# Optimization experiments

Hardware: AMD Instinct MI355X
Metric: run time of the kernel (lower is better)

The kernel has to match this reference:

```python
import jax, jax.numpy as jnp
from jax import lax
import numpy as np


def _chain(U, v, pos_seq):
    """Run the sequential Slater-determinant conditional-probability chain.
    U: (D, D) one-body density matrix P P^T.  v: (D, D) Jastrow matrix.
    pos_seq: (N,) int positions fed in order (replaces the sampling step,
    as in chainevaluate_amplitude).  Returns probs_all: (N, D).
    """
    D = U.shape[0]
    N = pos_seq.shape[0]
    diagU = jnp.diag(U)

    def step(carry, k):
        Xinv, Kpad, s = carry              # Xinv: (N,N) padded, Kpad: (N,) int, s: (D,)
        pos = pos_seq[k]
        # corr[pos'] = U[pos', K(:k)] @ Xinv(:k,:k) @ U[K(:k), pos']  for all pos'
        # padding is safe: rows/cols >= k of Xinv are zero.
        A = U[:, Kpad]                      # (D, N) gather of occupied columns
        corr = jnp.sum((A @ Xinv) * A, axis=1)          # (D,)
        unnorm = diagU - corr               # cond_prob_unnormalized (k=0: corr==0)
        probs_F = jnp.abs(unnorm / (N - k))  # Slater conditional prob
        probs_B = jnp.exp(-0.5 * s)          # Jastrow factor (k=0: s==0 -> ones)
        p = probs_F * probs_B
        probs = p / jnp.sum(p)
        # Sherman-Morrison rank-1 update of Xinv with the newly occupied site
        gg = 1.0 / unnorm[pos]
        uu = Xinv @ U[Kpad, pos]            # (N,)  zero beyond k
        vv = U[pos, Kpad] @ Xinv            # (N,)  (== uu since U symmetric)
        Xn = Xinv + gg * jnp.outer(uu, vv)
        Xn = Xn.at[k, :].set(-gg * vv)
        Xn = Xn.at[:, k].set(-gg * uu)
        Xn = Xn.at[k, k].set(gg)
        Kpad = Kpad.at[k].set(pos)
        s = s + v[:, pos]
        return (Xn, Kpad, s), probs

    init = (jnp.zeros((N, N), U.dtype), jnp.zeros((N,), jnp.int32), jnp.zeros((D,), U.dtype))
    _, probs_all = lax.scan(step, init, jnp.arange(N))
    return probs_all


def setup_inputs() -> dict:
    D, Np, B = 4096, 32, 8
    rng = np.random.default_rng(0)
    # orthonormal single-particle eigenfunctions (columns), as in the source model
    Q, _ = np.linalg.qr(rng.standard_normal((D, D)).astype(np.float64))
    eigfunc = jnp.asarray(Q, jnp.float32)
    vv = 0.01 * rng.standard_normal((D, D))
    v = jnp.asarray(0.5 * (vv + vv.T), jnp.float32)   # symmetric Jastrow matrix
    # strictly increasing occupied positions per batch (particle ordering)
    pos = np.stack([np.sort(rng.choice(D, size=Np, replace=False)) for _ in range(B)])
    positions = jnp.asarray(pos, jnp.int32)
    return {"eigfunc": eigfunc, "v": v, "positions": positions}


def reference(eigfunc, v, positions):
    Np = positions.shape[1]
    P = eigfunc[:, :Np]
    U = P @ P.T                              # (D, D)
    # vmap over independent sampling chains
    return jax.vmap(lambda ps: _chain(U, v, ps))(positions)   # (B, N, D)
```

## Files before the change

### kernel.cpp

```cpp
#include <hip/hip_runtime.h>
#include <math.h>

#define DD 4096
#define NP 32
#define BB 8
#define NBLK 16


__global__ __launch_bounds__(256, 1) void fused_kernel(const float* __restrict__ eig,
                                                       const float* __restrict__ v,
                                                       const int* __restrict__ pos,
                                                       float* __restrict__ out,
                                                       float* __restrict__ partial) {
    const int b = blockIdx.y;
    const int tid = threadIdx.x;
    const int d = blockIdx.x * 256 + tid;
    const int lane = tid & 63;
    const int wid = tid >> 6;
    const int r = lane & 31;

    __shared__ int ps[NP];
    __shared__ float Q[NP][36];
    __shared__ float wsum[4][NP];

    if (tid < NP) ps[tid] = pos[b * NP + tid];
    __syncthreads();

    float vv[NP];
#pragma unroll
    for (int k = 0; k < NP; k++) vv[k] = v[(size_t)ps[k] * DD + d];

    float a[NP];
    {
        const float4* arow = (const float4*)(eig + (size_t)ps[r] * DD);
#pragma unroll
        for (int i = 0; i < 8; i++) {
            float4 t = arow[i];
            a[4 * i] = t.x; a[4 * i + 1] = t.y; a[4 * i + 2] = t.z; a[4 * i + 3] = t.w;
        }
    }

    for (int k = 0; k < NP; k++) {
        float rk[NP];
#pragma unroll
        for (int i = 0; i < NP; i++) rk[i] = __shfl(a[i], k);
        float n0 = 0.f, n1 = 0.f;
#pragma unroll
        for (int i = 0; i < NP; i += 2) { n0 += rk[i] * rk[i]; n1 += rk[i + 1] * rk[i + 1]; }
        float inv = 1.0f / sqrtf(n0 + n1);
#pragma unroll
        for (int i = 0; i < NP; i++) rk[i] *= inv;
        float d0 = 0.f, d1 = 0.f;
#pragma unroll
        for (int i = 0; i < NP; i += 2) { d0 += a[i] * rk[i]; d1 += a[i + 1] * rk[i + 1]; }
        float f = (r > k) ? (d0 + d1) : 0.f;
#pragma unroll
        for (int i = 0; i < NP; i++) a[i] = (r == k) ? rk[i] : (a[i] - f * rk[i]);
    }

    float p[NP];
    {
        const float4* prow = (const float4*)(eig + (size_t)d * DD);
#pragma unroll
        for (int i = 0; i < 8; i++) {
            float4 t = prow[i];
            p[4 * i] = t.x; p[4 * i + 1] = t.y; p[4 * i + 2] = t.z; p[4 * i + 3] = t.w;
        }
    }

    float e[NP];
    {
        float s = 0.f;
#pragma unroll
        for (int k = 0; k < NP; k++) { e[k] = expf(-0.5f * s); s += vv[k]; }
    }

    float diagU = 0.f;
#pragma unroll
    for (int j = 0; j < NP; j++) diagU += p[j] * p[j];

    if (wid == 0 && lane < NP) {
        float4* qr = (float4*)&Q[lane][0];
#pragma unroll
        for (int i = 0; i < 8; i++) qr[i] = make_float4(a[4 * i], a[4 * i + 1], a[4 * i + 2], a[4 * i + 3]);
    }
    __syncthreads();

    float un = diagU;
#pragma unroll
    for (int k = 0; k < NP; k++) {
        float pr = fabsf(un) * (1.0f / (NP - k)) * e[k];
        out[((size_t)(b * NP + k)) * DD + d] = pr;
        float red = pr;
        red += __shfl_xor(red, 1);  red += __shfl_xor(red, 2);  red += __shfl_xor(red, 4);
        red += __shfl_xor(red, 8);  red += __shfl_xor(red, 16); red += __shfl_xor(red, 32);
        if (lane == 0) wsum[wid][k] = red;
        const float4* q4 = (const float4*)&Q[k][0];
        float acc0 = 0.f, acc1 = 0.f;
#pragma unroll
        for (int i = 0; i < 8; i += 2) {
            float4 qa = q4[i], qb = q4[i + 1];
            acc0 += qa.x * p[4 * i] + qa.y * p[4 * i + 1] + qa.z * p[4 * i + 2] + qa.w * p[4 * i + 3];
            acc1 += qb.x * p[4 * i + 4] + qb.y * p[4 * i + 5] + qb.z * p[4 * i + 6] + qb.w * p[4 * i + 7];
        }
        float t = acc0 + acc1;
        un -= t * t;
    }
    __syncthreads();
    if (tid < NP) {
        float sb = wsum[0][tid] + wsum[1][tid] + wsum[2][tid] + wsum[3][tid];
        partial[(size_t)(b * NP + tid) * NBLK + blockIdx.x] = sb;
    }
}

__global__ __launch_bounds__(256) void norm_kernel(float* __restrict__ out,
                                                   const float* __restrict__ partial) {
    int bk = blockIdx.x;
    __shared__ float invs;
    if (threadIdx.x == 0) {
        float s = 0.f;
        for (int i = 0; i < NBLK; i++) s += partial[bk * NBLK + i];
        invs = 1.0f / s;
    }
    __syncthreads();
    float iv = invs;
    float4* o = (float4*)(out + (size_t)bk * DD);
    for (int i = threadIdx.x; i < DD / 4; i += 256) {
        float4 x = o[i];
        x.x *= iv; x.y *= iv; x.z *= iv; x.w *= iv;
        o[i] = x;
    }
}

extern "C" void kernel_launch(void* const* d_in, const int* in_sizes, int n_in,
                              void* d_out, int out_size, void* d_ws, size_t ws_size,
                              hipStream_t stream) {
    const float* eig = (const float*)d_in[0];
    const float* v   = (const float*)d_in[1];
    const int*  pos  = (const int*)d_in[2];
    float* out = (float*)d_out;
    float* partial = (float*)d_ws;

    fused_kernel<<<dim3(NBLK, BB), 256, 0, stream>>>(eig, v, pos, out, partial);
    norm_kernel<<<dim3(BB * NP), 256, 0, stream>>>(out, partial);
}
```

Measured before the change: 43.39 us.

## Split Gram-Schmidt into separate kernel and widen chain grid to smaller blocks

Before, every block of the fused kernel redid the 32x32 Gram-Schmidt orthogonalization of the occupied rows. That work now runs once per batch in a small gs_kernel, which writes Q to workspace. The chain kernel loads Q from workspace and runs with 128-thread blocks over twice as many blocks, so more CUs are used. Its inner loop is restructured to compute all projections first, then probabilities, stores and reductions, and the norm kernel sums partials with a wave shuffle. The cost is an extra kernel launch and a serial dependency through global memory.

```diff
diff --git a/kernel.cpp b/kernel.cpp
--- a/kernel.cpp
+++ b/kernel.cpp
@@ -4,32 +4,19 @@
 #define DD 4096
 #define NP 32
 #define BB 8
-#define NBLK 16
+#define BT 128
+#define NBLK 32
 
 
-__global__ __launch_bounds__(256, 1) void fused_kernel(const float* __restrict__ eig,
-                                                       const float* __restrict__ v,
-                                                       const int* __restrict__ pos,
-                                                       float* __restrict__ out,
-                                                       float* __restrict__ partial) {
-    const int b = blockIdx.y;
+__global__ __launch_bounds__(64) void gs_kernel(const float* __restrict__ eig,
+                                                const int* __restrict__ pos,
+                                                float* __restrict__ Qws) {
+    const int b = blockIdx.x;
     const int tid = threadIdx.x;
-    const int d = blockIdx.x * 256 + tid;
-    const int lane = tid & 63;
-    const int wid = tid >> 6;
-    const int r = lane & 31;
-
+    const int r = tid & 31;
     __shared__ int ps[NP];
-    __shared__ float Q[NP][36];
-    __shared__ float wsum[4][NP];
-
     if (tid < NP) ps[tid] = pos[b * NP + tid];
     __syncthreads();
-
-    float vv[NP];
-#pragma unroll
-    for (int k = 0; k < NP; k++) vv[k] = v[(size_t)ps[k] * DD + d];
-
     float a[NP];
     {
         const float4* arow = (const float4*)(eig + (size_t)ps[r] * DD);
@@ -39,7 +26,6 @@
             a[4 * i] = t.x; a[4 * i + 1] = t.y; a[4 * i + 2] = t.z; a[4 * i + 3] = t.w;
         }
     }
-
     for (int k = 0; k < NP; k++) {
         float rk[NP];
 #pragma unroll
@@ -57,6 +43,36 @@
 #pragma unroll
         for (int i = 0; i < NP; i++) a[i] = (r == k) ? rk[i] : (a[i] - f * rk[i]);
     }
+    if (tid < NP) {
+        float4* q = (float4*)(Qws + ((size_t)b * NP + r) * NP);
+#pragma unroll
+        for (int i = 0; i < 8; i++)
+            q[i] = make_float4(a[4 * i], a[4 * i + 1], a[4 * i + 2], a[4 * i + 3]);
+    }
+}
+
+__global__ __launch_bounds__(BT, 1) void chain_kernel(const float* __restrict__ eig,
+                                                      const float* __restrict__ v,
+                                                      const int* __restrict__ pos,
+                                                      const float* __restrict__ Qws,
+                                                      float* __restrict__ out,
+                                                      float* __restrict__ partial) {
+    const int b = blockIdx.y;
+    const int tid = threadIdx.x;
+    const int d = blockIdx.x * BT + tid;
+    const int lane = tid & 63;
+    const int wid = tid >> 6;
+    __shared__ float Q[NP][NP];
+    __shared__ int ps[NP];
+    __shared__ float wsum[BT / 64][NP];
+    if (tid < NP) ps[tid] = pos[b * NP + tid];
+    {
+        const float4* src = (const float4*)(Qws + (size_t)b * NP * NP);
+        float4* dst = (float4*)&Q[0][0];
+        dst[tid] = src[tid];
+        dst[tid + BT] = src[tid + BT];
+    }
+    __syncthreads();
 
     float p[NP];
     {
@@ -67,64 +83,67 @@
             p[4 * i] = t.x; p[4 * i + 1] = t.y; p[4 * i + 2] = t.z; p[4 * i + 3] = t.w;
         }
     }
-
+    float vv[NP];
+#pragma unroll
+    for (int k = 0; k < NP; k++) vv[k] = v[(size_t)ps[k] * DD + d];
     float e[NP];
     {
         float s = 0.f;
 #pragma unroll
         for (int k = 0; k < NP; k++) { e[k] = expf(-0.5f * s); s += vv[k]; }
     }
-
     float diagU = 0.f;
 #pragma unroll
     for (int j = 0; j < NP; j++) diagU += p[j] * p[j];
 
-    if (wid == 0 && lane < NP) {
-        float4* qr = (float4*)&Q[lane][0];
+    float t[NP];
 #pragma unroll
-        for (int i = 0; i < 8; i++) qr[i] = make_float4(a[4 * i], a[4 * i + 1], a[4 * i + 2], a[4 * i + 3]);
+    for (int k = 0; k < NP; k++) {
+        const float4* q4 = (const float4*)&Q[k][0];
+        float a0 = 0.f, a1 = 0.f;
+#pragma unroll
+        for (int i = 0; i < 8; i += 2) {
+            float4 qa = q4[i], qb = q4[i + 1];
+            a0 += qa.x * p[4 * i]     + qa.y * p[4 * i + 1] + qa.z * p[4 * i + 2] + qa.w * p[4 * i + 3];
+            a1 += qb.x * p[4 * i + 4] + qb.y * p[4 * i + 5] + qb.z * p[4 * i + 6] + qb.w * p[4 * i + 7];
+        }
+        t[k] = a0 + a1;
     }
-    __syncthreads();
-
+    float pr[NP];
     float un = diagU;
 #pragma unroll
     for (int k = 0; k < NP; k++) {
-        float pr = fabsf(un) * (1.0f / (NP - k)) * e[k];
-        out[((size_t)(b * NP + k)) * DD + d] = pr;
-        float red = pr;
+        pr[k] = fabsf(un) * (1.0f / (NP - k)) * e[k];
+        un -= t[k] * t[k];
+    }
+#pragma unroll
+    for (int k = 0; k < NP; k++) out[((size_t)(b * NP + k)) * DD + d] = pr[k];
+#pragma unroll
+    for (int k = 0; k < NP; k++) {
+        float red = pr[k];
         red += __shfl_xor(red, 1);  red += __shfl_xor(red, 2);  red += __shfl_xor(red, 4);
         red += __shfl_xor(red, 8);  red += __shfl_xor(red, 16); red += __shfl_xor(red, 32);
         if (lane == 0) wsum[wid][k] = red;
-        const float4* q4 = (const float4*)&Q[k][0];
-        float acc0 = 0.f, acc1 = 0.f;
-#pragma unroll
-        for (int i = 0; i < 8; i += 2) {
-            float4 qa = q4[i], qb = q4[i + 1];
-            acc0 += qa.x * p[4 * i] + qa.y * p[4 * i + 1] + qa.z * p[4 * i + 2] + qa.w * p[4 * i + 3];
-            acc1 += qb.x * p[4 * i + 4] + qb.y * p[4 * i + 5] + qb.z * p[4 * i + 6] + qb.w * p[4 * i + 7];
-        }
-        float t = acc0 + acc1;
-        un -= t * t;
     }
     __syncthreads();
-    if (tid < NP) {
-        float sb = wsum[0][tid] + wsum[1][tid] + wsum[2][tid] + wsum[3][tid];
-        partial[(size_t)(b * NP + tid) * NBLK + blockIdx.x] = sb;
-    }
+    if (tid < NP)
+        partial[((size_t)(b * NP + tid)) * NBLK + blockIdx.x] = wsum[0][tid] + wsum[1][tid];
 }
 
 __global__ __launch_bounds__(256) void norm_kernel(float* __restrict__ out,
                                                    const float* __restrict__ partial) {
-    int bk = blockIdx.x;
+    const int bk = blockIdx.x;
     __shared__ float invs;
-    if (threadIdx.x == 0) {
-        float s = 0.f;
-        for (int i = 0; i < NBLK; i++) s += partial[bk * NBLK + i];
-        invs = 1.0f / s;
+    if (threadIdx.x < 64) {
+        float s = (threadIdx.x < NBLK) ? partial[(size_t)bk * NBLK + threadIdx.x] : 0.f;
+        s += __shfl_xor(s, 1);  s += __shfl_xor(s, 2);  s += __shfl_xor(s, 4);
+        s += __shfl_xor(s, 8);  s += __shfl_xor(s, 16); s += __shfl_xor(s, 32);
+        if (threadIdx.x == 0) invs = 1.0f / s;
     }
     __syncthreads();
-    float iv = invs;
+    const float iv = invs;
     float4* o = (float4*)(out + (size_t)bk * DD);
+#pragma unroll
     for (int i = threadIdx.x; i < DD / 4; i += 256) {
         float4 x = o[i];
         x.x *= iv; x.y *= iv; x.z *= iv; x.w *= iv;
@@ -139,8 +158,11 @@
     const float* v   = (const float*)d_in[1];
     const int*  pos  = (const int*)d_in[2];
     float* out = (float*)d_out;
-    float* partial = (float*)d_ws;
+    float* ws  = (float*)d_ws;
+    float* Qws     = ws;
+    float* partial = Qws + BB * NP * NP;
 
-    fused_kernel<<<dim3(NBLK, BB), 256, 0, stream>>>(eig, v, pos, out, partial);
+    gs_kernel<<<dim3(BB), 64, 0, stream>>>(eig, pos, Qws);
+    chain_kernel<<<dim3(NBLK, BB), BT, 0, stream>>>(eig, v, pos, Qws, out, partial);
     norm_kernel<<<dim3(BB * NP), 256, 0, stream>>>(out, partial);
 }
```

Result: faster. 41.96 us (-3.3%).
